# Kernel optimization log

Measured on AMD Instinct MI355X. Metric: run time of the kernel, lower is better.

The kernel has to match this reference:

```python
import jax, jax.numpy as jnp
import numpy as np

B, T, N1, N2, D, H, DH = 8, 4, 1024, 64, 1024, 16, 64
INNER = H * DH
EPS = 1e-5


def layernorm(x, g, b):
    mu = jnp.mean(x, axis=-1, keepdims=True)
    var = jnp.var(x, axis=-1, keepdims=True)
    return (x - mu) * jax.lax.rsqrt(var + EPS) * g + b


def setup_inputs() -> dict:
    key = jax.random.key(0)
    ks = jax.random.split(key, 8)
    s = 0.02
    return {
        "x": jax.random.normal(ks[0], (B, T, N1, D), jnp.float32),
        "latents": jax.random.normal(ks[1], (B, T, N2, D), jnp.float32),
        "gm": jnp.ones((D,), jnp.float32),
        "bm": jnp.zeros((D,), jnp.float32),
        "gl": jnp.ones((D,), jnp.float32),
        "bl": jnp.zeros((D,), jnp.float32),
        "Wq": jax.random.normal(ks[2], (D, INNER), jnp.float32) * s,
        "Wkv": jax.random.normal(ks[3], (D, 2 * INNER), jnp.float32) * s,
        "Wout": jax.random.normal(ks[4], (INNER, D), jnp.float32) * s,
        "Wd1": jax.random.normal(ks[5], (D, D // 4), jnp.float32) * s,
        "bd1": jnp.zeros((D // 4,), jnp.float32),
        "Wd2": jax.random.normal(ks[6], (D // 4, H), jnp.float32) * s,
        "bd2": jnp.zeros((H,), jnp.float32),
    }


def reference(x, latents, gm, bm, gl, bl, Wq, Wkv, Wout, Wd1, bd1, Wd2, bd2):
    b, t, n1, d = x.shape
    n2 = latents.shape[2]
    h, dh = H, DH
    scale = dh ** -0.5

    xn = layernorm(x, gm, bm)
    ln = layernorm(latents, gl, bl)

    # q: (b, h, t, n2, dh)
    q = (ln @ Wq).reshape(b, t, n2, h, dh).transpose(0, 3, 1, 2, 4)
    # kv over image tokens + first latent token -> nk = n1 + 1
    kv_in = jnp.concatenate([xn, ln[:, :, 0:1]], axis=2)
    nk = n1 + 1
    kv = (kv_in @ Wkv).reshape(b, t, nk, 2, h, dh)
    k = kv[:, :, :, 0].transpose(0, 3, 1, 2, 4)  # (b, h, t, nk, dh)
    v = kv[:, :, :, 1].transpose(0, 3, 1, 2, 4)

    sim = jnp.einsum('bhtid,bhtjd->bhtij', q * scale, k)
    sim = sim - jax.lax.stop_gradient(jnp.max(sim, axis=-1, keepdims=True))
    attn = jax.nn.softmax(sim, axis=-1)

    # dynamic per-head weights from mean-pooled (normed) latents: (b, t, h)
    hid = jax.nn.relu(ln.mean(axis=2) @ Wd1 + bd1)
    dw = jax.nn.softmax(hid @ Wd2 + bd2, axis=-1)
    attn = attn * dw.transpose(0, 2, 1)[:, :, :, None, None]  # (b,h,t,1,1)

    out = jnp.einsum('bhtij,bhtjd->bhtid', attn, v)
    out = out.transpose(0, 2, 3, 1, 4).reshape(b, t, n2, h * dh)
    return out @ Wout
```

## Files before the change

### kernel.cpp

```cpp
#include <hip/hip_runtime.h>
#include <cstdint>
#include <cstddef>

constexpr int CB = 8, CT = 4, CN1 = 1024, CN2 = 64, CD = 1024, CH = 16, CDH = 64;
constexpr int CBT = CB * CT;
constexpr int CNK = CN1 + 1;
constexpr int CINNER = CH * CDH;

__device__ __forceinline__ unsigned short f2bf(float f) {
  union { float f; unsigned int u; } v; v.f = f;
  unsigned int u = v.u;
  u += 0x7fffu + ((u >> 16) & 1u);
  return (unsigned short)(u >> 16);
}

typedef __attribute__((ext_vector_type(8))) short short8;
typedef __attribute__((ext_vector_type(8))) __bf16 bf16x8;
typedef __attribute__((ext_vector_type(4))) float floatx4;

template <typename V>
__device__ __forceinline__ auto mfma_bf16_impl(V a, V b, floatx4 c, int)
    -> decltype(__builtin_amdgcn_mfma_f32_16x16x32_bf16(a, b, c, 0, 0, 0)) {
  return __builtin_amdgcn_mfma_f32_16x16x32_bf16(a, b, c, 0, 0, 0);
}
template <typename V>
__device__ __forceinline__ floatx4 mfma_bf16_impl(V a, V b, floatx4 c, long) {
  return __builtin_amdgcn_mfma_f32_16x16x32_bf16(
      __builtin_bit_cast(bf16x8, a), __builtin_bit_cast(bf16x8, b), c, 0, 0, 0);
}
__device__ __forceinline__ floatx4 mfma_bf16(short8 a, short8 b, floatx4 c) {
  return mfma_bf16_impl(a, b, c, 0);
}

#if __has_builtin(__builtin_amdgcn_global_load_lds)
#define HAS_GLDS 1
__device__ __forceinline__ void glds16(const unsigned short* g, unsigned short* l) {
  __builtin_amdgcn_global_load_lds(
      (const __attribute__((address_space(1))) void*)g,
      (__attribute__((address_space(3))) void*)l, 16, 0, 0);
}
#else
#define HAS_GLDS 0
#endif

__global__ __launch_bounds__(256) void ln_kernel(
    const float* __restrict__ x, const float* __restrict__ g,
    const float* __restrict__ b, unsigned short* __restrict__ obf,
    float* __restrict__ of32) {
  const int row = blockIdx.x * 4 + (threadIdx.x >> 6);
  const int lane = threadIdx.x & 63;
  const float4* xr = (const float4*)(x + (size_t)row * CD);
  float4 v[4];
#pragma unroll
  for (int k = 0; k < 4; ++k) v[k] = xr[lane + 64 * k];
  float s = 0.f, s2 = 0.f;
#pragma unroll
  for (int k = 0; k < 4; ++k) {
    s  += v[k].x + v[k].y + v[k].z + v[k].w;
    s2 += v[k].x*v[k].x + v[k].y*v[k].y + v[k].z*v[k].z + v[k].w*v[k].w;
  }
#pragma unroll
  for (int off = 32; off; off >>= 1) { s += __shfl_xor(s, off); s2 += __shfl_xor(s2, off); }
  const float mean = s * (1.0f / 1024.0f);
  const float var  = s2 * (1.0f / 1024.0f) - mean * mean;
  const float rstd = rsqrtf(var + 1e-5f);
#pragma unroll
  for (int k = 0; k < 4; ++k) {
    const float4 gv = ((const float4*)g)[lane + 64 * k];
    const float4 bv = ((const float4*)b)[lane + 64 * k];
    float4 y;
    y.x = (v[k].x - mean) * rstd * gv.x + bv.x;
    y.y = (v[k].y - mean) * rstd * gv.y + bv.y;
    y.z = (v[k].z - mean) * rstd * gv.z + bv.z;
    y.w = (v[k].w - mean) * rstd * gv.w + bv.w;
    ushort4 o; o.x = f2bf(y.x); o.y = f2bf(y.y); o.z = f2bf(y.z); o.w = f2bf(y.w);
    ((ushort4*)(obf + (size_t)row * CD))[lane + 64 * k] = o;
    if (of32) ((float4*)(of32 + (size_t)row * CD))[lane + 64 * k] = y;
  }
}

__global__ __launch_bounds__(256) void wtrans_kernel(
    const float* __restrict__ W, unsigned short* __restrict__ WT, int K, int N) {
  __shared__ float t[64][65];
  const int n0 = blockIdx.x * 64, k0 = blockIdx.y * 64;
  const int tid = threadIdx.x;
  const int kr = tid >> 4, ns = (tid & 15) * 4;
#pragma unroll
  for (int i = 0; i < 4; ++i) {
    const int k = kr + i * 16;
    const float4 v = *(const float4*)&W[(size_t)(k0 + k) * N + n0 + ns];
    t[k][ns + 0] = v.x; t[k][ns + 1] = v.y; t[k][ns + 2] = v.z; t[k][ns + 3] = v.w;
  }
  __syncthreads();
  const int n = tid >> 2, ks = (tid & 3) * 16;
#pragma unroll
  for (int c = 0; c < 4; ++c) {
    ushort4 o;
    o.x = f2bf(t[ks + c * 4 + 0][n]);
    o.y = f2bf(t[ks + c * 4 + 1][n]);
    o.z = f2bf(t[ks + c * 4 + 2][n]);
    o.w = f2bf(t[ks + c * 4 + 3][n]);
    *(ushort4*)&WT[(size_t)(n0 + n) * K + k0 + ks + c * 4] = o;
  }
}

template <bool A_KV, bool C_BF16>
__global__ __launch_bounds__(256) void gemm128_kernel(
    const unsigned short* __restrict__ A, const unsigned short* __restrict__ xn,
    const unsigned short* __restrict__ lnb, const unsigned short* __restrict__ BT,
    unsigned short* __restrict__ Cb, float* __restrict__ Cf,
    int M, int N, int K) {
  __shared__ __attribute__((aligned(16))) unsigned short As[128 * 32];
  __shared__ __attribute__((aligned(16))) unsigned short Bs[128 * 32];
  const int tid = threadIdx.x;
  const int col0 = blockIdx.x * 128, row0 = blockIdx.y * 128;
  const int srow = tid >> 2, skseg = (tid & 3) * 8;

  auto arow_ptr = [&](int grow) -> const unsigned short* {
    if (grow >= M) grow = M - 1;
    if (A_KV) {
      const int bt = grow / CNK, j = grow - bt * CNK;
      return (j < CN1) ? xn + ((size_t)(bt * CN1 + j)) * K + skseg
                       : lnb + ((size_t)(bt * CN2)) * K + skseg;
    }
    return A + (size_t)grow * K + skseg;
  };
  const unsigned short* a0 = arow_ptr(row0 + srow);
  const unsigned short* a1 = arow_ptr(row0 + 64 + srow);
  const unsigned short* b0 = BT + (size_t)(col0 + srow) * K + skseg;
  const unsigned short* b1 = BT + (size_t)(col0 + 64 + srow) * K + skseg;

  const int lane = tid & 63, wave = tid >> 6;
  const int wrow = (wave >> 1) * 64, wcol = (wave & 1) * 64;
  const int i16 = lane & 15, quad = lane >> 4;

  floatx4 acc[4][4] = {};
  for (int kt = 0; kt < K; kt += 32) {
    __syncthreads();
#if HAS_GLDS
    glds16(a0 + kt, &As[tid * 8]);
    glds16(a1 + kt, &As[2048 + tid * 8]);
    glds16(b0 + kt, &Bs[tid * 8]);
    glds16(b1 + kt, &Bs[2048 + tid * 8]);
#else
    *(uint4*)&As[tid * 8]        = *(const uint4*)(a0 + kt);
    *(uint4*)&As[2048 + tid * 8] = *(const uint4*)(a1 + kt);
    *(uint4*)&Bs[tid * 8]        = *(const uint4*)(b0 + kt);
    *(uint4*)&Bs[2048 + tid * 8] = *(const uint4*)(b1 + kt);
#endif
    __syncthreads();
    short8 af[4], bf[4];
#pragma unroll
    for (int ti = 0; ti < 4; ++ti)
      af[ti] = *(const short8*)&As[(wrow + ti * 16 + i16) * 32 + quad * 8];
#pragma unroll
    for (int tj = 0; tj < 4; ++tj)
      bf[tj] = *(const short8*)&Bs[(wcol + tj * 16 + i16) * 32 + quad * 8];
#pragma unroll
    for (int ti = 0; ti < 4; ++ti)
#pragma unroll
      for (int tj = 0; tj < 4; ++tj)
        acc[ti][tj] = mfma_bf16(af[ti], bf[tj], acc[ti][tj]);
  }
#pragma unroll
  for (int ti = 0; ti < 4; ++ti)
#pragma unroll
    for (int tj = 0; tj < 4; ++tj) {
      const int gc = col0 + wcol + tj * 16 + i16;
#pragma unroll
      for (int r = 0; r < 4; ++r) {
        const int gr = row0 + wrow + ti * 16 + quad * 4 + r;
        if (gr < M) {
          if (C_BF16) Cb[(size_t)gr * N + gc] = f2bf(acc[ti][tj][r]);
          else        Cf[(size_t)gr * N + gc] = acc[ti][tj][r];
        }
      }
    }
}

template <bool A_KV>
__global__ __launch_bounds__(512, 2) void gemmkv_kernel(
    const unsigned short* __restrict__ xn, const unsigned short* __restrict__ lnb,
    const unsigned short* __restrict__ BT, unsigned short* __restrict__ Cb,
    int M, int N, int K) {
  __shared__ __attribute__((aligned(16))) unsigned short As[3 * 8192];
  const int tid = threadIdx.x;
  const int mb = blockIdx.x >> 3, nb = blockIdx.x & 7;
  const int row0 = mb * 256, col0 = nb * 256;

  auto arow = [&](int grow) -> const unsigned short* {
    if (grow >= M) grow = M - 1;
    if (A_KV) {
      const int bt = grow / CNK, j = grow - bt * CNK;
      return (j < CN1) ? xn + ((size_t)(bt * CN1 + j)) * K
                       : lnb + ((size_t)(bt * CN2)) * K;
    }
    return (const unsigned short*)nullptr;
  };
  const int c0 = tid, c1 = tid + 512;
  const int rA0 = c0 >> 2, sA0 = (c0 & 3) ^ ((rA0 >> 1) & 3);
  const int rA1 = c1 >> 2, sA1 = (c1 & 3) ^ ((rA1 >> 1) & 3);
  const unsigned short* pA0 = arow(row0 + rA0) + sA0 * 8;
  const unsigned short* pA1 = arow(row0 + rA1) + sA1 * 8;

  auto stage = [&](int s) {
    const int sb = (s % 3) * 8192;
#if HAS_GLDS
    glds16(pA0 + s * 32, &As[sb + tid * 8]);
    glds16(pA1 + s * 32, &As[sb + 4096 + tid * 8]);
#else
    *(uint4*)&As[sb + tid * 8]        = *(const uint4*)(pA0 + s * 32);
    *(uint4*)&As[sb + 4096 + tid * 8] = *(const uint4*)(pA1 + s * 32);
#endif
  };

  const int lane = tid & 63, wave = tid >> 6;
  const int wr = wave >> 2, wc = wave & 3;
  const int i16 = lane & 15, quad = lane >> 4;
  int offA[8];
#pragma unroll
  for (int ti = 0; ti < 8; ++ti) {
    const int r = wr * 128 + ti * 16 + i16;
    offA[ti] = r * 32 + (quad ^ ((r >> 1) & 3)) * 8;
  }
  const unsigned short* pB[4];
#pragma unroll
  for (int tj = 0; tj < 4; ++tj) {
    const int col = col0 + wc * 64 + tj * 16 + i16;
    pB[tj] = BT + (size_t)col * K + quad * 8;
  }

  floatx4 acc[8][4] = {};
  short8 bfA[4], bfB[4];

  stage(0); stage(1);
  __builtin_amdgcn_sched_barrier(0);
#pragma unroll
  for (int tj = 0; tj < 4; ++tj) bfA[tj] = *(const short8*)(pB[tj]);
  __builtin_amdgcn_sched_barrier(0);

  auto phase = [&](int s, short8 (&bfC)[4], short8 (&bfN)[4], bool preB, bool doStage) {
    const unsigned short* Asl = &As[(s % 3) * 8192];
    if (preB) {
#pragma unroll
      for (int tj = 0; tj < 4; ++tj)
        bfN[tj] = *(const short8*)(pB[tj] + (s + 1) * 32);
    }
    __builtin_amdgcn_sched_barrier(0);
    short8 af[8];
#pragma unroll
    for (int ti = 0; ti < 8; ++ti) af[ti] = *(const short8*)(Asl + offA[ti]);
    if (doStage) stage(s + 2);
    __builtin_amdgcn_sched_barrier(0);
    __builtin_amdgcn_s_setprio(1);
#pragma unroll
    for (int ti = 0; ti < 8; ++ti)
#pragma unroll
      for (int tj = 0; tj < 4; ++tj)
        acc[ti][tj] = mfma_bf16(af[ti], bfC[tj], acc[ti][tj]);
    __builtin_amdgcn_s_setprio(0);
  };

  const int NSL = K >> 5;
  for (int s = 0; s < NSL; s += 2) {
    asm volatile("s_waitcnt vmcnt(6)" ::: "memory");
    __builtin_amdgcn_s_barrier();
    __builtin_amdgcn_sched_barrier(0);
    phase(s, bfA, bfB, true, s + 2 < NSL);
    if (s + 1 == NSL - 1) { asm volatile("s_waitcnt vmcnt(4)" ::: "memory"); }
    else                  { asm volatile("s_waitcnt vmcnt(6)" ::: "memory"); }
    __builtin_amdgcn_s_barrier();
    __builtin_amdgcn_sched_barrier(0);
    phase(s + 1, bfB, bfA, s + 2 < NSL, s + 3 < NSL);
  }

#pragma unroll
  for (int ti = 0; ti < 8; ++ti)
#pragma unroll
    for (int tj = 0; tj < 4; ++tj) {
      const int gc = col0 + wc * 64 + tj * 16 + i16;
#pragma unroll
      for (int r = 0; r < 4; ++r) {
        const int gr = row0 + wr * 128 + ti * 16 + quad * 4 + r;
        if (gr < M) Cb[(size_t)gr * N + gc] = f2bf(acc[ti][tj][r]);
      }
    }
}

__global__ __launch_bounds__(256) void dwmean_kernel(
    const float* __restrict__ lnf, float* __restrict__ meanp) {
  const int bt = blockIdx.x >> 2, dseg = blockIdx.x & 3;
  const int d = dseg * 256 + threadIdx.x;
  const float* base = lnf + (size_t)bt * CN2 * CD + d;
  float s = 0.f;
#pragma unroll 4
  for (int r = 0; r < CN2; ++r) s += base[(size_t)r * CD];
  meanp[bt * CD + d] = s * (1.0f / 64.0f);
}

__global__ __launch_bounds__(256) void dwmlp_kernel(
    const float* __restrict__ meanp, const float* __restrict__ Wd1,
    const float* __restrict__ bd1, float* __restrict__ hidp) {
  __shared__ float red[8][32];
  const int bt = blockIdx.x >> 3, og = blockIdx.x & 7;
  const int o = threadIdx.x & 31, seg = threadIdx.x >> 5;
  const int col = og * 32 + o;
  const float* mb = meanp + bt * CD;
  float s = 0.f;
#pragma unroll 4
  for (int d = seg * 128; d < seg * 128 + 128; ++d)
    s += mb[d] * Wd1[(size_t)d * 256 + col];
  red[seg][o] = s;
  __syncthreads();
  if (seg == 0) {
    float t = red[0][o];
#pragma unroll
    for (int k = 1; k < 8; ++k) t += red[k][o];
    hidp[bt * 256 + col] = fmaxf(t + bd1[col], 0.0f);
  }
}

__global__ __launch_bounds__(256) void dwfin_kernel(
    const float* __restrict__ hidp, const float* __restrict__ Wd2,
    const float* __restrict__ bd2, float* __restrict__ dw) {
  __shared__ float red[16][16];
  __shared__ float lg[16];
  const int bt = blockIdx.x;
  const int h = threadIdx.x & 15, seg = threadIdx.x >> 4;
  const float* hb = hidp + bt * 256;
  float s = 0.f;
#pragma unroll
  for (int o = seg * 16; o < seg * 16 + 16; ++o)
    s += hb[o] * Wd2[o * 16 + h];
  red[seg][h] = s;
  __syncthreads();
  if (seg == 0) {
    float t = red[0][h];
#pragma unroll
    for (int k = 1; k < 16; ++k) t += red[k][h];
    lg[h] = t + bd2[h];
  }
  __syncthreads();
  if (threadIdx.x < 16) {
    float mx = lg[0];
#pragma unroll
    for (int k = 1; k < 16; ++k) mx = fmaxf(mx, lg[k]);
    float sum = 0.f;
#pragma unroll
    for (int k = 0; k < 16; ++k) sum += __expf(lg[k] - mx);
    dw[bt * 16 + threadIdx.x] = __expf(lg[threadIdx.x] - mx) / sum;
  }
}

__global__ __launch_bounds__(256) void attn_kernel(
    const unsigned short* __restrict__ Q,
    const unsigned short* __restrict__ KV,
    const float* __restrict__ dw,
    unsigned short* __restrict__ AO) {
  __shared__ __attribute__((aligned(16))) unsigned short ks[2][64 * 72];
  __shared__ __attribute__((aligned(16))) unsigned short vt[2][64 * 72];
  const int raw = blockIdx.x;
  const int bt = (raw & 7) * 4 + ((raw >> 3) >> 4);
  const int h  = (raw >> 3) & 15;
  const int tid = threadIdx.x;
  const int lane = tid & 63, wave = tid >> 6;
  const int i16 = lane & 15, quad = lane >> 4;
  const int wrow = wave * 16;

  const unsigned short* qbase =
      Q + ((size_t)(bt * 64 + wrow + i16)) * CINNER + h * 64;
  const short8 bq0 = *(const short8*)(qbase + quad * 8);
  const short8 bq1 = *(const short8*)(qbase + 32 + quad * 8);

  const int jrb = tid & 31, seg = tid >> 5;
  const int t_ = jrb & 15, hlf_ = jrb >> 4;
  const int vcol0 = ((t_ >> 2) << 3) + (t_ & 3) + 4 * hlf_;
  const unsigned short* kvb = KV + ((size_t)bt * CNK) * 2048 + h * 64 + seg * 8;

  uint4 kk[2], vv[2];
  auto load_tile = [&](int j0) {
#pragma unroll
    for (int c = 0; c < 2; ++c) {
      const int j = j0 + c * 32 + jrb;
      if (j < CNK) {
        const unsigned short* p = kvb + (size_t)j * 2048;
        kk[c] = *(const uint4*)p;
        vv[c] = *(const uint4*)(p + 1024);
      } else {
        kk[c] = make_uint4(0, 0, 0, 0);
        vv[c] = make_uint4(0, 0, 0, 0);
      }
    }
  };
  auto write_tile = [&](int buf) {
#pragma unroll
    for (int c = 0; c < 2; ++c) {
      const int jr = c * 32 + jrb;
      *(uint4*)&ks[buf][jr * 72 + seg * 8] = kk[c];
      const int vcol = c * 32 + vcol0;
      const unsigned int w[4] = {vv[c].x, vv[c].y, vv[c].z, vv[c].w};
#pragma unroll
      for (int p = 0; p < 4; ++p) {
        vt[buf][(seg * 8 + 2 * p + 0) * 72 + vcol] = (unsigned short)(w[p] & 0xffffu);
        vt[buf][(seg * 8 + 2 * p + 1) * 72 + vcol] = (unsigned short)(w[p] >> 16);
      }
    }
  };

  float l = 0.f;
  floatx4 O[4] = {{0,0,0,0}, {0,0,0,0}, {0,0,0,0}, {0,0,0,0}};
  const float expC = 0.18033688011112042f;

  load_tile(0);
  write_tile(0);
  constexpr int NT = 17;
  for (int t = 0; t < NT; ++t) {
    if (t + 1 < NT) load_tile((t + 1) * 64);
    __syncthreads();
    const int buf = t & 1;
    const unsigned short* ksb = ks[buf];
    const unsigned short* vtb = vt[buf];
#pragma unroll
    for (int c = 0; c < 2; ++c) {
      floatx4 s0 = {0,0,0,0}, s1 = {0,0,0,0};
      const short8 a00 = *(const short8*)&ksb[((2*c)   * 16 + i16) * 72 + quad * 8];
      const short8 a01 = *(const short8*)&ksb[((2*c)   * 16 + i16) * 72 + 32 + quad * 8];
      const short8 a10 = *(const short8*)&ksb[((2*c+1) * 16 + i16) * 72 + quad * 8];
      const short8 a11 = *(const short8*)&ksb[((2*c+1) * 16 + i16) * 72 + 32 + quad * 8];
      s0 = mfma_bf16(a00, bq0, s0); s0 = mfma_bf16(a01, bq1, s0);
      s1 = mfma_bf16(a10, bq0, s1); s1 = mfma_bf16(a11, bq1, s1);
      unsigned short pb0[4], pb1[4];
      if (t == NT - 1) {
#pragma unroll
        for (int r = 0; r < 4; ++r) {
          const int k0g = t * 64 + (2*c)   * 16 + quad * 4 + r;
          const int k1g = t * 64 + (2*c+1) * 16 + quad * 4 + r;
          const float p0 = (k0g < CNK) ? exp2f(s0[r] * expC) : 0.f;
          const float p1 = (k1g < CNK) ? exp2f(s1[r] * expC) : 0.f;
          l += p0 + p1;
          pb0[r] = f2bf(p0); pb1[r] = f2bf(p1);
        }
      } else {
#pragma unroll
        for (int r = 0; r < 4; ++r) {
          const float p0 = exp2f(s0[r] * expC);
          const float p1 = exp2f(s1[r] * expC);
          l += p0 + p1;
          pb0[r] = f2bf(p0); pb1[r] = f2bf(p1);
        }
      }
      const short8 bp = {
          (short)pb0[0], (short)pb0[1], (short)pb0[2], (short)pb0[3],
          (short)pb1[0], (short)pb1[1], (short)pb1[2], (short)pb1[3]};
#pragma unroll
      for (int dt = 0; dt < 4; ++dt) {
        const short8 av = *(const short8*)&vtb[(dt * 16 + i16) * 72 + c * 32 + quad * 8];
        O[dt] = mfma_bf16(av, bp, O[dt]);
      }
    }
    if (t + 1 < NT) write_tile((t + 1) & 1);
  }

  l += __shfl_xor(l, 16);
  l += __shfl_xor(l, 32);
  const float wsc = dw[bt * 16 + h] / l;
  unsigned short* obase = AO + ((size_t)(bt * 64 + wrow + i16)) * CINNER + h * 64;
#pragma unroll
  for (int dt = 0; dt < 4; ++dt)
#pragma unroll
    for (int r = 0; r < 4; ++r)
      obase[dt * 16 + quad * 4 + r] = f2bf(O[dt][r] * wsc);
}

extern "C" void kernel_launch(void* const* d_in, const int* in_sizes, int n_in,
                              void* d_out, int out_size, void* d_ws, size_t ws_size,
                              hipStream_t stream) {
  const float* x       = (const float*)d_in[0];
  const float* latents = (const float*)d_in[1];
  const float* gm  = (const float*)d_in[2];
  const float* bm  = (const float*)d_in[3];
  const float* gl  = (const float*)d_in[4];
  const float* bl  = (const float*)d_in[5];
  const float* Wq  = (const float*)d_in[6];
  const float* Wkv = (const float*)d_in[7];
  const float* Wout= (const float*)d_in[8];
  const float* Wd1 = (const float*)d_in[9];
  const float* bd1 = (const float*)d_in[10];
  const float* Wd2 = (const float*)d_in[11];
  const float* bd2 = (const float*)d_in[12];
  float* out = (float*)d_out;

  char* ws = (char*)d_ws;
  size_t off = 0;
  auto alloc = [&](size_t bytes) -> void* {
    void* p = ws + off;
    off += (bytes + 255) & ~(size_t)255;
    return p;
  };
  unsigned short* xn   = (unsigned short*)alloc((size_t)CBT * CN1 * CD * 2);
  unsigned short* kv   = (unsigned short*)alloc((size_t)CBT * CNK * 2048 * 2);
  float*          lnf  = (float*)        alloc((size_t)CBT * CN2 * CD * 4);
  unsigned short* lnb  = (unsigned short*)alloc((size_t)CBT * CN2 * CD * 2);
  unsigned short* wqT  = (unsigned short*)alloc((size_t)CD * CINNER * 2);
  unsigned short* wkvT = (unsigned short*)alloc((size_t)CD * 2 * CINNER * 2);
  unsigned short* woT  = (unsigned short*)alloc((size_t)CINNER * CD * 2);
  unsigned short* qb   = (unsigned short*)alloc((size_t)CBT * CN2 * CINNER * 2);
  unsigned short* aob  = (unsigned short*)alloc((size_t)CBT * CN2 * CINNER * 2);
  float*          dwp  = (float*)        alloc((size_t)CBT * CH * 4);
  float*          meanp= (float*)        alloc((size_t)CBT * CD * 4);
  float*          hidp = (float*)        alloc((size_t)CBT * 256 * 4);
  if (off > ws_size) return;

  ln_kernel<<<CBT * CN1 / 4, 256, 0, stream>>>(x, gm, bm, xn, nullptr);
  ln_kernel<<<CBT * CN2 / 4, 256, 0, stream>>>(latents, gl, bl, lnb, lnf);
  wtrans_kernel<<<dim3(CINNER / 64, CD / 64), 256, 0, stream>>>(Wq, wqT, CD, CINNER);
  wtrans_kernel<<<dim3(2 * CINNER / 64, CD / 64), 256, 0, stream>>>(Wkv, wkvT, CD, 2 * CINNER);
  wtrans_kernel<<<dim3(CD / 64, CINNER / 64), 256, 0, stream>>>(Wout, woT, CINNER, CD);
  gemm128_kernel<false, true><<<dim3(1024 / 128, 2048 / 128), 256, 0, stream>>>(
      lnb, nullptr, nullptr, wqT, qb, nullptr, 2048, 1024, 1024);
  {
    const int MB = (CBT * CNK + 255) / 256;
    gemmkv_kernel<true><<<MB * 8, 512, 0, stream>>>(
        xn, lnb, wkvT, kv, CBT * CNK, 2048, 1024);
  }
  dwmean_kernel<<<CBT * 4, 256, 0, stream>>>(lnf, meanp);
  dwmlp_kernel<<<CBT * 8, 256, 0, stream>>>(meanp, Wd1, bd1, hidp);
  dwfin_kernel<<<CBT, 256, 0, stream>>>(hidp, Wd2, bd2, dwp);
  attn_kernel<<<CBT * CH, 256, 0, stream>>>(qb, kv, dwp, aob);
  gemm128_kernel<false, false><<<dim3(1024 / 128, 2048 / 128), 256, 0, stream>>>(
      aob, nullptr, nullptr, woT, nullptr, out, 2048, 1024, 1024);
}
```

Before: 602.4 us.

## Rewrite KV GEMM as 8-phase pipeline staging both A and B through LDS

The KV projection GEMM now stages both the activation and the weight tiles into double-buffered LDS with a K-step of 64, replacing the old version that read B directly from global memory into registers. Each K-tile is split into eight quarter-phases that interleave LDS reads, async global-to-LDS loads and MFMA blocks, separated by barriers. The goal is to hide global latency and cut redundant B traffic across waves. The cost is more LDS per block (64KB, which may limit occupancy to two blocks) and many more barriers per tile.

```diff
diff --git a/kernel.cpp b/kernel.cpp
--- a/kernel.cpp
+++ b/kernel.cpp
@@ -42,6 +42,11 @@
 #else
 #define HAS_GLDS 0
 #endif
+
+#define FENCEV(n) asm volatile("s_waitcnt vmcnt(" #n ")" ::: "memory")
+#define SBAR __builtin_amdgcn_s_barrier()
+#define LGKM0 do { asm volatile("s_waitcnt lgkmcnt(0)" ::: "memory"); \
+                   __builtin_amdgcn_sched_barrier(0); } while (0)
 
 __global__ __launch_bounds__(256) void ln_kernel(
     const float* __restrict__ x, const float* __restrict__ g,
@@ -179,11 +184,12 @@
 }
 
 template <bool A_KV>
-__global__ __launch_bounds__(512, 2) void gemmkv_kernel(
+__global__ __launch_bounds__(512, 2) void gemm8p_kernel(
     const unsigned short* __restrict__ xn, const unsigned short* __restrict__ lnb,
     const unsigned short* __restrict__ BT, unsigned short* __restrict__ Cb,
     int M, int N, int K) {
-  __shared__ __attribute__((aligned(16))) unsigned short As[3 * 8192];
+  __shared__ __attribute__((aligned(16))) unsigned short As[2][2][128 * 64];
+  __shared__ __attribute__((aligned(16))) unsigned short Bs[2][2][128 * 64];
   const int tid = threadIdx.x;
   const int mb = blockIdx.x >> 3, nb = blockIdx.x & 7;
   const int row0 = mb * 256, col0 = nb * 256;
@@ -197,92 +203,147 @@
     }
     return (const unsigned short*)nullptr;
   };
-  const int c0 = tid, c1 = tid + 512;
-  const int rA0 = c0 >> 2, sA0 = (c0 & 3) ^ ((rA0 >> 1) & 3);
-  const int rA1 = c1 >> 2, sA1 = (c1 & 3) ^ ((rA1 >> 1) & 3);
-  const unsigned short* pA0 = arow(row0 + rA0) + sA0 * 8;
-  const unsigned short* pA1 = arow(row0 + rA1) + sA1 * 8;
-
-  auto stage = [&](int s) {
-    const int sb = (s % 3) * 8192;
+
+  const int rr0 = tid >> 3;
+  const int sl  = (tid & 7) ^ (rr0 & 7);
+  const unsigned short* pA[2][2];
+  const unsigned short* pB[2][2];
+#pragma unroll
+  for (int h = 0; h < 2; ++h)
+#pragma unroll
+    for (int c = 0; c < 2; ++c) {
+      pA[h][c] = arow(row0 + h * 128 + rr0 + c * 64) + sl * 8;
+      pB[h][c] = BT + (size_t)(col0 + h * 128 + rr0 + c * 64) * K + sl * 8;
+    }
+
+  auto stageA = [&](int buf, int h, int t) {
+    unsigned short* d = &As[buf][h][tid * 8];
 #if HAS_GLDS
-    glds16(pA0 + s * 32, &As[sb + tid * 8]);
-    glds16(pA1 + s * 32, &As[sb + 4096 + tid * 8]);
+    glds16(pA[h][0] + t * 64, d);
+    glds16(pA[h][1] + t * 64, d + 4096);
 #else
-    *(uint4*)&As[sb + tid * 8]        = *(const uint4*)(pA0 + s * 32);
-    *(uint4*)&As[sb + 4096 + tid * 8] = *(const uint4*)(pA1 + s * 32);
+    *(uint4*)d          = *(const uint4*)(pA[h][0] + t * 64);
+    *(uint4*)(d + 4096) = *(const uint4*)(pA[h][1] + t * 64);
+#endif
+  };
+  auto stageB = [&](int buf, int h, int t) {
+    unsigned short* d = &Bs[buf][h][tid * 8];
+#if HAS_GLDS
+    glds16(pB[h][0] + t * 64, d);
+    glds16(pB[h][1] + t * 64, d + 4096);
+#else
+    *(uint4*)d          = *(const uint4*)(pB[h][0] + t * 64);
+    *(uint4*)(d + 4096) = *(const uint4*)(pB[h][1] + t * 64);
 #endif
   };
 
   const int lane = tid & 63, wave = tid >> 6;
   const int wr = wave >> 2, wc = wave & 3;
   const int i16 = lane & 15, quad = lane >> 4;
-  int offA[8];
-#pragma unroll
-  for (int ti = 0; ti < 8; ++ti) {
-    const int r = wr * 128 + ti * 16 + i16;
-    offA[ti] = r * 32 + (quad ^ ((r >> 1) & 3)) * 8;
-  }
-  const unsigned short* pB[4];
-#pragma unroll
-  for (int tj = 0; tj < 4; ++tj) {
-    const int col = col0 + wc * 64 + tj * 16 + i16;
-    pB[tj] = BT + (size_t)col * K + quad * 8;
-  }
-
+  const int sw = i16 & 7;
+  const int slk0 = (quad ^ sw) * 8;
+  const int slk1 = ((4 + quad) ^ sw) * 8;
+  const int brow = (wc & 1) * 64;
+
+  short8 aA[8], bB[8];
   floatx4 acc[8][4] = {};
-  short8 bfA[4], bfB[4];
-
-  stage(0); stage(1);
-  __builtin_amdgcn_sched_barrier(0);
-#pragma unroll
-  for (int tj = 0; tj < 4; ++tj) bfA[tj] = *(const short8*)(pB[tj]);
-  __builtin_amdgcn_sched_barrier(0);
-
-  auto phase = [&](int s, short8 (&bfC)[4], short8 (&bfN)[4], bool preB, bool doStage) {
-    const unsigned short* Asl = &As[(s % 3) * 8192];
-    if (preB) {
-#pragma unroll
-      for (int tj = 0; tj < 4; ++tj)
-        bfN[tj] = *(const short8*)(pB[tj] + (s + 1) * 32);
-    }
-    __builtin_amdgcn_sched_barrier(0);
-    short8 af[8];
-#pragma unroll
-    for (int ti = 0; ti < 8; ++ti) af[ti] = *(const short8*)(Asl + offA[ti]);
-    if (doStage) stage(s + 2);
-    __builtin_amdgcn_sched_barrier(0);
+
+  auto readA4 = [&](const unsigned short* Ah, int mlo) {
+#pragma unroll
+    for (int i = 0; i < 4; ++i) {
+      const int base = ((mlo + i) * 16 + i16) * 64;
+      aA[i * 2 + 0] = *(const short8*)(Ah + base + slk0);
+      aA[i * 2 + 1] = *(const short8*)(Ah + base + slk1);
+    }
+  };
+  auto readB2 = [&](const unsigned short* Bh, int nlo) {
+#pragma unroll
+    for (int j = 0; j < 2; ++j) {
+      const int base = (brow + (nlo + j) * 16 + i16) * 64;
+      bB[(nlo + j) * 2 + 0] = *(const short8*)(Bh + base + slk0);
+      bB[(nlo + j) * 2 + 1] = *(const short8*)(Bh + base + slk1);
+    }
+  };
+  auto mfmaQ = [&](int mlo, int nlo) {
     __builtin_amdgcn_s_setprio(1);
 #pragma unroll
-    for (int ti = 0; ti < 8; ++ti)
-#pragma unroll
-      for (int tj = 0; tj < 4; ++tj)
-        acc[ti][tj] = mfma_bf16(af[ti], bfC[tj], acc[ti][tj]);
+    for (int i = 0; i < 4; ++i)
+#pragma unroll
+      for (int j = 0; j < 2; ++j) {
+        acc[mlo + i][nlo + j] =
+            mfma_bf16(aA[i * 2 + 0], bB[(nlo + j) * 2 + 0], acc[mlo + i][nlo + j]);
+        acc[mlo + i][nlo + j] =
+            mfma_bf16(aA[i * 2 + 1], bB[(nlo + j) * 2 + 1], acc[mlo + i][nlo + j]);
+      }
     __builtin_amdgcn_s_setprio(0);
   };
 
-  const int NSL = K >> 5;
-  for (int s = 0; s < NSL; s += 2) {
-    asm volatile("s_waitcnt vmcnt(6)" ::: "memory");
-    __builtin_amdgcn_s_barrier();
-    __builtin_amdgcn_sched_barrier(0);
-    phase(s, bfA, bfB, true, s + 2 < NSL);
-    if (s + 1 == NSL - 1) { asm volatile("s_waitcnt vmcnt(4)" ::: "memory"); }
-    else                  { asm volatile("s_waitcnt vmcnt(6)" ::: "memory"); }
-    __builtin_amdgcn_s_barrier();
-    __builtin_amdgcn_sched_barrier(0);
-    phase(s + 1, bfB, bfA, s + 2 < NSL, s + 3 < NSL);
-  }
-
-#pragma unroll
-  for (int ti = 0; ti < 8; ++ti)
-#pragma unroll
-    for (int tj = 0; tj < 4; ++tj) {
-      const int gc = col0 + wc * 64 + tj * 16 + i16;
+  stageB(0, 0, 0); stageA(0, 0, 0); stageB(0, 1, 0); stageA(0, 1, 0);
+  stageB(1, 0, 1); stageA(1, 0, 1);
+  FENCEV(4);
+  SBAR;
+
+  const unsigned short* A0 = &As[0][wr][0];
+  const unsigned short* B0 = &Bs[0][wc >> 1][0];
+  const unsigned short* A1 = &As[1][wr][0];
+  const unsigned short* B1 = &Bs[1][wc >> 1][0];
+
+  auto iter = [&](int t, bool full) {
+    readB2(B0, 0); readA4(A0, 0);
+    stageB(1, 1, t + 1);
+    SBAR; LGKM0;
+    mfmaQ(0, 0);
+    SBAR;
+    readB2(B0, 2);
+    stageA(1, 1, t + 1);
+    SBAR; LGKM0;
+    mfmaQ(0, 2);
+    SBAR;
+    readA4(A0, 4);
+    if (full) stageB(0, 0, t + 2);
+    SBAR; LGKM0;
+    mfmaQ(4, 0);
+    SBAR;
+    if (full) stageA(0, 0, t + 2);
+    SBAR;
+    mfmaQ(4, 2);
+    if (full) { FENCEV(4); } else { FENCEV(0); }
+    SBAR;
+    readB2(B1, 0); readA4(A1, 0);
+    if (full) stageB(0, 1, t + 2);
+    SBAR; LGKM0;
+    mfmaQ(0, 0);
+    SBAR;
+    readB2(B1, 2);
+    if (full) stageA(0, 1, t + 2);
+    SBAR; LGKM0;
+    mfmaQ(0, 2);
+    SBAR;
+    readA4(A1, 4);
+    if (full) stageB(1, 0, t + 3);
+    SBAR; LGKM0;
+    mfmaQ(4, 0);
+    SBAR;
+    if (full) stageA(1, 0, t + 3);
+    SBAR;
+    mfmaQ(4, 2);
+    if (full) FENCEV(4);
+    SBAR;
+  };
+
+  const int NT = K >> 6;
+  for (int t = 0; t + 2 < NT; t += 2) iter(t, true);
+  iter(NT - 2, false);
+
+#pragma unroll
+  for (int m = 0; m < 8; ++m)
+#pragma unroll
+    for (int n = 0; n < 4; ++n) {
+      const int gc = col0 + wc * 64 + n * 16 + i16;
 #pragma unroll
       for (int r = 0; r < 4; ++r) {
-        const int gr = row0 + wr * 128 + ti * 16 + quad * 4 + r;
-        if (gr < M) Cb[(size_t)gr * N + gc] = f2bf(acc[ti][tj][r]);
+        const int gr = row0 + wr * 128 + m * 16 + quad * 4 + r;
+        if (gr < M) Cb[(size_t)gr * N + gc] = f2bf(acc[m][n][r]);
       }
     }
 }
@@ -520,7 +581,7 @@
       lnb, nullptr, nullptr, wqT, qb, nullptr, 2048, 1024, 1024);
   {
     const int MB = (CBT * CNK + 255) / 256;
-    gemmkv_kernel<true><<<MB * 8, 512, 0, stream>>>(
+    gemm8p_kernel<true><<<MB * 8, 512, 0, stream>>>(
         xn, lnb, wkvT, kv, CBT * CNK, 2048, 1024);
   }
   dwmean_kernel<<<CBT * 4, 256, 0, stream>>>(lnf, meanp);
```

Result: faster. 550.6 us (-8.6%).
